# Kernel tuning notes

Measured on AMD Instinct MI355X. Metric: run time of the kernel, lower is better.

The kernel has to match this reference:

```python
import jax, jax.numpy as jnp
import numpy as np

B, N, K, S_IN, S_OUT, C, FD = 32, 325, 20, 12, 12, 10, 64
ALPHA = 0.5  # LeakyReLU negative slope

def leaky(x):
    return jnp.where(x >= 0, x, ALPHA * x)

def setup_inputs() -> dict:
    key = jax.random.key(0)
    ks = jax.random.split(key, 9)
    s = 0.2
    return {
        "fushed_features": jax.random.normal(ks[0], (B, N, FD), jnp.float32),
        "input_data": jax.random.normal(ks[1], (B, N, S_IN), jnp.float32),
        "w_W": jax.random.normal(ks[2], (S_IN, S_OUT), jnp.float32) * s,
        "w_b": jax.random.normal(ks[3], (S_OUT,), jnp.float32) * s,
        "a1_W": jax.random.normal(ks[4], (2 * S_OUT, 4 * S_OUT), jnp.float32) * s,
        "a1_b": jax.random.normal(ks[5], (4 * S_OUT,), jnp.float32) * s,
        "a2_W": jax.random.normal(ks[6], (4 * S_OUT, C), jnp.float32) * s,
        "a2_b": jax.random.normal(ks[7], (C,), jnp.float32) * s,
        "adj_mx_topk_index": jax.random.randint(ks[8], (B, N, K), 0, N),
    }

def reference(fushed_features, input_data, w_W, w_b, a1_W, a1_b, a2_W, a2_b, adj_mx_topk_index):
    # w_net: Linear + LeakyReLU -> wh [B,N,S_OUT]
    wh = leaky(input_data @ w_W + w_b)
    # a_net on cat([wh_i, wh_j]): split first linear to avoid materializing [B,N,N,2*S_OUT]
    hx = wh @ a1_W[:S_OUT]   # contribution of wh_x (row node i)
    hy = wh @ a1_W[S_OUT:]   # contribution of wh_y (col node j)
    hidden = leaky(hx[:, :, None, :] + hy[:, None, :, :] + a1_b)   # [B,N,N,4*S_OUT]
    attention = leaky(hidden @ a2_W + a2_b)                        # [B,N,N,C]
    idx = adj_mx_topk_index                                        # [B,N,K]
    # gather top-k neighbors along dim 2
    idx_c = jnp.broadcast_to(idx[..., None], idx.shape + (attention.shape[-1],))
    attention_mask = jnp.take_along_axis(attention, idx_c, axis=2)  # [B,N,K,C]
    attention_mask = jax.nn.softmax(attention_mask, axis=-1)
    # gather neighbor features: wh_expand_top_k[b,i,k] = wh[b, idx[b,i,k]]
    wh_topk = wh[jnp.arange(wh.shape[0])[:, None, None], idx]       # [B,N,K,S_OUT]
    # output = attention_mask^T @ wh_topk
    output_data = jnp.einsum('bnkc,bnks->bncs', attention_mask, wh_topk)
    # clustering loss on detached neighbor features (cosine similarity)
    wt = jax.lax.stop_gradient(wh_topk)
    wtn = wt / (jnp.linalg.norm(wt, axis=-1, keepdims=True) + 1e-8)
    dist_mat = jnp.einsum('bnks,bnls->bnkl', wtn, wtn)              # [B,N,K,K]
    same = (dist_mat >= 0.5).astype(dist_mat.dtype)
    diff = 1.0 - same
    prob = jnp.einsum('bnkc,bnlc->bnkl', attention_mask, attention_mask)
    prob = jnp.clip(prob, 1e-4, 1.0 - 1e-4)
    logp = jnp.log(prob)
    cl = -(same * logp - diff * logp)
    cluster_loss = (cl.sum((-1, -2)) - jnp.trace(cl, axis1=-2, axis2=-1)).mean()
    return output_data, cluster_loss, dist_mat.mean(), wh.mean()
```

## Files before the change

kernel.cpp:

```cpp
#include <hip/hip_runtime.h>
#include <math.h>

#define Bdim 32
#define Ndim 325
#define Kdim 20
#define Sdim 12
#define Cdim 10
#define Hdim 48
#define NB   (Bdim*Ndim)
#define OUT_SCALARS (NB*Cdim*Sdim)
#define Tpairs (Kdim*(Kdim-1)/2)
#define BN_BLOCKS (NB/4)
#define NODE_BLOCKS 260
#define NPB 40

#define O_WH  0
#define O_HX  (O_WH + NB*Sdim)
#define O_HY  (O_HX + NB*Hdim)
#define O_PCL (O_HY + NB*Hdim)
#define O_PDS (O_PCL + BN_BLOCKS)
#define O_PWH (O_PDS + BN_BLOCKS)
#define WS_BASE_FLOATS (O_PWH + NODE_BLOCKS)

__device__ __forceinline__ float leaky(float x) { return x >= 0.f ? x : 0.5f * x; }

__global__ __launch_bounds__(256)
void node_kernel(const float* __restrict__ x,
                 const float* __restrict__ wW, const float* __restrict__ wb,
                 const float* __restrict__ A1, const float* __restrict__ b1,
                 float* __restrict__ ws)
{
    __shared__ float s_wh[NPB][Sdim];
    __shared__ float s_r[4];
    const int tid = threadIdx.x;
    const int base = blockIdx.x * NPB;

    float v = 0.f;
    #pragma unroll
    for (int rep = 0; rep < 2; rep++) {
        const int e = tid + rep * 256;
        if (e < NPB * Sdim) {
            const int n = e / Sdim, s = e - n * Sdim;
            const float* xr = x + (size_t)(base + n) * Sdim;
            float acc = wb[s];
            #pragma unroll
            for (int i = 0; i < Sdim; i++) acc += xr[i] * wW[i * Sdim + s];
            acc = leaky(acc);
            s_wh[n][s] = acc;
            ws[O_WH + (size_t)(base + n) * Sdim + s] = acc;
            v += acc;
        }
    }
    __syncthreads();

    #pragma unroll
    for (int rep = 0; rep < 15; rep++) {
        const int e = tid + rep * 256;
        const int n = e / 96, r = e - n * 96;
        const int which = r / Hdim, d = r - which * Hdim;
        const float4 w0 = *(const float4*)&s_wh[n][0];
        const float4 w1 = *(const float4*)&s_wh[n][4];
        const float4 w2 = *(const float4*)&s_wh[n][8];
        const float* Ac = A1 + (which * Sdim) * Hdim + d;
        float acc = which ? 0.f : b1[d];
        acc += w0.x*Ac[0*Hdim] + w0.y*Ac[1*Hdim] + w0.z*Ac[2*Hdim] + w0.w*Ac[3*Hdim]
             + w1.x*Ac[4*Hdim] + w1.y*Ac[5*Hdim] + w1.z*Ac[6*Hdim] + w1.w*Ac[7*Hdim]
             + w2.x*Ac[8*Hdim] + w2.y*Ac[9*Hdim] + w2.z*Ac[10*Hdim] + w2.w*Ac[11*Hdim];
        ws[(which ? O_HY : O_HX) + (size_t)(base + n) * Hdim + d] = acc;
    }

    #pragma unroll
    for (int off = 32; off > 0; off >>= 1) v += __shfl_down(v, off);
    if ((tid & 63) == 0) s_r[tid >> 6] = v;
    __syncthreads();
    if (tid == 0) ws[O_PWH + blockIdx.x] = s_r[0] + s_r[1] + s_r[2] + s_r[3];
}

__global__ __launch_bounds__(256)
void mega_kernel(const int* __restrict__ topk,
                 const float* __restrict__ A2, const float* __restrict__ b2,
                 float* __restrict__ ws, float* __restrict__ out)
{
    __shared__ float s_A2  [Hdim * Cdim];
    __shared__ float s_whj [4][Kdim][12];
    __shared__ float s_am  [4][Kdim][12];
    __shared__ float s_invn[4][Kdim];
    __shared__ float s_red[2][4];

    const int tid = threadIdx.x;
    const int slot = tid >> 6, t = tid & 63;

    if (tid < 120) *(float4*)&s_A2[tid * 4] = *(const float4*)&A2[tid * 4];
    __syncthreads();

    if (tid < 160) {
        const int e = tid >> 1, half = tid & 1;
        const int gid = blockIdx.x * 80 + e;
        const int bn_e = gid / Kdim;
        const int b_e  = bn_e / Ndim;
        const int j    = topk[gid];
        const int ek   = e / 20, kk = e - ek * 20;

        const float4* hx4 = (const float4*)(ws + O_HX + (size_t)bn_e * Hdim) + half * 6;
        const float4* hy4 = (const float4*)(ws + O_HY + ((size_t)b_e * Ndim + j) * Hdim) + half * 6;

        float acc[Cdim];
        #pragma unroll
        for (int c = 0; c < Cdim; c++) acc[c] = 0.f;
        #pragma unroll
        for (int q = 0; q < 6; q++) {
            const float4 xv = hx4[q], yv = hy4[q];
            const float hh[4] = { leaky(xv.x + yv.x), leaky(xv.y + yv.y),
                                  leaky(xv.z + yv.z), leaky(xv.w + yv.w) };
            #pragma unroll
            for (int i = 0; i < 4; i++) {
                const int d = half * 24 + q * 4 + i;
                #pragma unroll
                for (int c = 0; c < Cdim; c++)
                    acc[c] += hh[i] * s_A2[d * Cdim + c];
            }
        }
        float full[Cdim];
        #pragma unroll
        for (int c = 0; c < Cdim; c++) full[c] = acc[c] + __shfl_xor(acc[c], 1);
        if (half == 0) {
            float m = -1e30f;
            #pragma unroll
            for (int c = 0; c < Cdim; c++) { full[c] = leaky(full[c] + b2[c]); m = fmaxf(m, full[c]); }
            float sum = 0.f;
            #pragma unroll
            for (int c = 0; c < Cdim; c++) { full[c] = __expf(full[c] - m); sum += full[c]; }
            const float inv = 1.f / sum;
            *(float4*)&s_am[ek][kk][0] = make_float4(full[0]*inv, full[1]*inv, full[2]*inv, full[3]*inv);
            *(float4*)&s_am[ek][kk][4] = make_float4(full[4]*inv, full[5]*inv, full[6]*inv, full[7]*inv);
            *(float4*)&s_am[ek][kk][8] = make_float4(full[8]*inv, full[9]*inv, 0.f, 0.f);
        }
    } else {
        for (int i = tid - 160; i < 240; i += 96) {
            const int kf = i / 3, q = i - kf * 3;
            const int sl = kf / 20, k = kf - sl * 20;
            const int gidx = blockIdx.x * 80 + kf;
            const int bn_i = gidx / Kdim;
            const int b_i  = bn_i / Ndim;
            const int j    = topk[gidx];
            const float4 v = *(const float4*)(ws + O_WH + ((size_t)b_i * Ndim + j) * Sdim + q * 4);
            *(float4*)&s_whj[sl][k][q * 4] = v;
        }
    }
    __syncthreads();

    const int bn = blockIdx.x * 4 + slot;
    float cl = 0.f, ds = 0.f;

    if (t < Kdim) {
        const float4 w0 = *(const float4*)&s_whj[slot][t][0];
        const float4 w1 = *(const float4*)&s_whj[slot][t][4];
        const float4 w2 = *(const float4*)&s_whj[slot][t][8];
        const float nn = w0.x*w0.x + w0.y*w0.y + w0.z*w0.z + w0.w*w0.w
                       + w1.x*w1.x + w1.y*w1.y + w1.z*w1.z + w1.w*w1.w
                       + w2.x*w2.x + w2.y*w2.y + w2.z*w2.z + w2.w*w2.w;
        const float invn = 1.f / (sqrtf(nn) + 1e-8f);
        s_invn[slot][t] = invn;
        ds += nn * invn * invn;
    } else if (t < Kdim + 30) {
        const int e = t - Kdim, c = e / 3, sq = e - c * 3;
        float4 o = make_float4(0.f, 0.f, 0.f, 0.f);
        #pragma unroll
        for (int k = 0; k < Kdim; k++) {
            const float a = s_am[slot][k][c];
            const float4 w = *(const float4*)&s_whj[slot][k][sq * 4];
            o.x += a * w.x; o.y += a * w.y; o.z += a * w.z; o.w += a * w.w;
        }
        *(float4*)(out + (size_t)bn * (Cdim * Sdim) + c * Sdim + sq * 4) = o;
    }
    __builtin_amdgcn_wave_barrier();

    #pragma unroll
    for (int it = 0; it < 3; it++) {
        const int e = t + it * 64;
        if (e < Tpairs) {
            const int r = Tpairs - 1 - e;
            const int m = (int)((sqrtf((float)(8 * r + 1)) - 1.f) * 0.5f + 1e-4f);
            const int k = Kdim - 2 - m;
            const int l = Kdim - 1 - (r - (m * (m + 1)) / 2);

            const float4 a0 = *(const float4*)&s_whj[slot][k][0];
            const float4 a1 = *(const float4*)&s_whj[slot][k][4];
            const float4 a2 = *(const float4*)&s_whj[slot][k][8];
            const float4 c0 = *(const float4*)&s_whj[slot][l][0];
            const float4 c1 = *(const float4*)&s_whj[slot][l][4];
            const float4 c2 = *(const float4*)&s_whj[slot][l][8];
            const float draw = a0.x*c0.x + a0.y*c0.y + a0.z*c0.z + a0.w*c0.w
                             + a1.x*c1.x + a1.y*c1.y + a1.z*c1.z + a1.w*c1.w
                             + a2.x*c2.x + a2.y*c2.y + a2.z*c2.z + a2.w*c2.w;
            const float d = draw * s_invn[slot][k] * s_invn[slot][l];

            const float4 p0 = *(const float4*)&s_am[slot][k][0];
            const float4 p1 = *(const float4*)&s_am[slot][k][4];
            const float4 p2 = *(const float4*)&s_am[slot][k][8];
            const float4 q0 = *(const float4*)&s_am[slot][l][0];
            const float4 q1 = *(const float4*)&s_am[slot][l][4];
            const float4 q2 = *(const float4*)&s_am[slot][l][8];
            float p = p0.x*q0.x + p0.y*q0.y + p0.z*q0.z + p0.w*q0.w
                    + p1.x*q1.x + p1.y*q1.y + p1.z*q1.z + p1.w*q1.w
                    + p2.x*q2.x + p2.y*q2.y + p2.z*q2.z + p2.w*q2.w;

            p = fminf(fmaxf(p, 1e-4f), 1.f - 1e-4f);
            const float lp = __logf(p);
            ds += 2.f * d;
            cl += 2.f * ((d >= 0.5f) ? -lp : lp);
        }
    }

    #pragma unroll
    for (int off = 32; off > 0; off >>= 1) {
        cl += __shfl_down(cl, off);
        ds += __shfl_down(ds, off);
    }
    if (t == 0) { s_red[0][slot] = cl; s_red[1][slot] = ds; }
    __syncthreads();
    if (tid == 0) {
        ws[O_PCL + blockIdx.x] = s_red[0][0] + s_red[0][1] + s_red[0][2] + s_red[0][3];
        ws[O_PDS + blockIdx.x] = s_red[1][0] + s_red[1][1] + s_red[1][2] + s_red[1][3];
    }
}

__global__ __launch_bounds__(1024)
void finalize(const float* __restrict__ ws, float* __restrict__ out)
{
    const int t = threadIdx.x;
    float cl = 0.f, ds = 0.f, wm = 0.f;
    for (int i = t; i < BN_BLOCKS; i += 1024) {
        cl += ws[O_PCL + i]; ds += ws[O_PDS + i];
    }
    if (t < NODE_BLOCKS) wm = ws[O_PWH + t];
    #pragma unroll
    for (int off = 32; off > 0; off >>= 1) {
        cl += __shfl_down(cl, off);
        ds += __shfl_down(ds, off);
        wm += __shfl_down(wm, off);
    }
    __shared__ float r[3][16];
    const int w = t >> 6, lane = t & 63;
    if (lane == 0) { r[0][w] = cl; r[1][w] = ds; r[2][w] = wm; }
    __syncthreads();
    if (t == 0) {
        float c = 0.f, d = 0.f, m = 0.f;
        #pragma unroll
        for (int i = 0; i < 16; i++) { c += r[0][i]; d += r[1][i]; m += r[2][i]; }
        out[OUT_SCALARS + 0] = c * (1.f / (float)NB);
        out[OUT_SCALARS + 1] = d * (1.f / ((float)NB * Kdim * Kdim));
        out[OUT_SCALARS + 2] = m * (1.f / ((float)NB * Sdim));
    }
}

__global__ void zero_scalars(float* out) {
    const int t = threadIdx.x;
    if (t < 3) out[OUT_SCALARS + t] = 0.f;
}

__global__ __launch_bounds__(64)
void fused_kernel(const float* __restrict__ input_data,
                  const float* __restrict__ w_W,  const float* __restrict__ w_b,
                  const float* __restrict__ a1_W, const float* __restrict__ a1_b,
                  const float* __restrict__ a2_W, const float* __restrict__ a2_b,
                  const int*   __restrict__ topk,
                  float* __restrict__ out)
{
    __shared__ float s_wW[Sdim * Sdim];
    __shared__ float s_wb[Sdim];
    __shared__ float s_A1[2 * Sdim * Hdim];
    __shared__ float s_b1[Hdim];
    __shared__ float s_A2f[Hdim * Cdim];
    __shared__ float s_b2f[Cdim];
    __shared__ float s_whs[Sdim];
    __shared__ float s_hx[Hdim];
    __shared__ float s_whj[Kdim][Sdim + 1];
    __shared__ float s_hid[Kdim][Hdim + 1];
    __shared__ float s_am [Kdim][Cdim + 1];
    __shared__ float s_wtn[Kdim][Sdim + 1];
    __shared__ int   s_idx[Kdim];

    const int t = threadIdx.x, bn = blockIdx.x, b = bn / Ndim;

    for (int i = t; i < Sdim * Sdim; i += 64)      s_wW[i] = w_W[i];
    if (t < Sdim)                                  s_wb[t] = w_b[t];
    for (int i = t; i < 2 * Sdim * Hdim; i += 64)  s_A1[i] = a1_W[i];
    if (t < Hdim)                                  s_b1[t] = a1_b[t];
    for (int i = t; i < Hdim * Cdim; i += 64)      s_A2f[i] = a2_W[i];
    if (t < Cdim)                                  s_b2f[t] = a2_b[t];
    if (t < Kdim)                                  s_idx[t] = topk[(size_t)bn * Kdim + t];
    __syncthreads();

    const float* xs = input_data + (size_t)bn * Sdim;
    if (t < Sdim) {
        float acc = s_wb[t];
        #pragma unroll
        for (int i = 0; i < Sdim; i++) acc += xs[i] * s_wW[i * Sdim + t];
        s_whs[t] = leaky(acc);
    }
    __syncthreads();

    if (t < Hdim) {
        float acc = 0.f;
        #pragma unroll
        for (int s = 0; s < Sdim; s++) acc += s_whs[s] * s_A1[s * Hdim + t];
        s_hx[t] = acc;
    }
    for (int e = t; e < Kdim * Sdim; e += 64) {
        const int k = e / Sdim, ss = e - k * Sdim;
        const float* xj = input_data + ((size_t)b * Ndim + s_idx[k]) * Sdim;
        float acc = s_wb[ss];
        #pragma unroll
        for (int i = 0; i < Sdim; i++) acc += xj[i] * s_wW[i * Sdim + ss];
        s_whj[k][ss] = leaky(acc);
    }
    __syncthreads();

    for (int e = t; e < Kdim * Hdim; e += 64) {
        const int k = e / Hdim, d = e - k * Hdim;
        float acc = s_hx[d] + s_b1[d];
        #pragma unroll
        for (int s = 0; s < Sdim; s++) acc += s_whj[k][s] * s_A1[(Sdim + s) * Hdim + d];
        s_hid[k][d] = leaky(acc);
    }
    __syncthreads();

    for (int e = t; e < Kdim * Cdim; e += 64) {
        const int k = e / Cdim, c = e - k * Cdim;
        float acc = s_b2f[c];
        #pragma unroll
        for (int d = 0; d < Hdim; d++) acc += s_hid[k][d] * s_A2f[d * Cdim + c];
        s_am[k][c] = leaky(acc);
    }
    __syncthreads();

    if (t < Kdim) {
        float m = -1e30f;
        #pragma unroll
        for (int c = 0; c < Cdim; c++) m = fmaxf(m, s_am[t][c]);
        float ex[Cdim]; float sum = 0.f;
        #pragma unroll
        for (int c = 0; c < Cdim; c++) { ex[c] = expf(s_am[t][c] - m); sum += ex[c]; }
        const float inv = 1.f / sum;
        #pragma unroll
        for (int c = 0; c < Cdim; c++) s_am[t][c] = ex[c] * inv;
        float nn = 0.f;
        #pragma unroll
        for (int s = 0; s < Sdim; s++) nn += s_whj[t][s] * s_whj[t][s];
        const float invn = 1.f / (sqrtf(nn) + 1e-8f);
        #pragma unroll
        for (int s = 0; s < Sdim; s++) s_wtn[t][s] = s_whj[t][s] * invn;
    }
    __syncthreads();

    float* op = out + (size_t)bn * (Cdim * Sdim);
    for (int e = t; e < Cdim * Sdim; e += 64) {
        const int c = e / Sdim, ss = e - c * Sdim;
        float acc = 0.f;
        #pragma unroll
        for (int k = 0; k < Kdim; k++) acc += s_am[k][c] * s_whj[k][ss];
        op[e] = acc;
    }

    float cl = 0.f, ds = 0.f;
    for (int e = t; e < Kdim * Kdim; e += 64) {
        const int k = e / Kdim, l = e - k * Kdim;
        float d = 0.f;
        #pragma unroll
        for (int s = 0; s < Sdim; s++) d += s_wtn[k][s] * s_wtn[l][s];
        ds += d;
        if (k != l) {
            float p = 0.f;
            #pragma unroll
            for (int c = 0; c < Cdim; c++) p += s_am[k][c] * s_am[l][c];
            p = fminf(fmaxf(p, 1e-4f), 1.f - 1e-4f);
            const float lp = logf(p);
            cl += (d >= 0.5f) ? -lp : lp;
        }
    }
    float whl = (t < Sdim) ? s_whs[t] : 0.f;
    #pragma unroll
    for (int off = 32; off > 0; off >>= 1) {
        cl  += __shfl_down(cl,  off);
        ds  += __shfl_down(ds,  off);
        whl += __shfl_down(whl, off);
    }
    if (t == 0) {
        atomicAdd(&out[OUT_SCALARS + 0], cl  * (1.f / (float)NB));
        atomicAdd(&out[OUT_SCALARS + 1], ds  * (1.f / ((float)NB * Kdim * Kdim)));
        atomicAdd(&out[OUT_SCALARS + 2], whl * (1.f / ((float)NB * Sdim)));
    }
}

extern "C" void kernel_launch(void* const* d_in, const int* in_sizes, int n_in,
                              void* d_out, int out_size, void* d_ws, size_t ws_size,
                              hipStream_t stream) {
    (void)in_sizes; (void)n_in; (void)out_size;
    const float* input_data = (const float*)d_in[1];
    const float* w_W  = (const float*)d_in[2];
    const float* w_b  = (const float*)d_in[3];
    const float* a1_W = (const float*)d_in[4];
    const float* a1_b = (const float*)d_in[5];
    const float* a2_W = (const float*)d_in[6];
    const float* a2_b = (const float*)d_in[7];
    const int*   topk = (const int*)d_in[8];
    float* out = (float*)d_out;
    float* ws  = (float*)d_ws;

    if (ws_size >= (size_t)WS_BASE_FLOATS * sizeof(float)) {
        hipLaunchKernelGGL(node_kernel, dim3(NODE_BLOCKS), dim3(256), 0, stream,
                           input_data, w_W, w_b, a1_W, a1_b, ws);
        hipLaunchKernelGGL(mega_kernel, dim3(BN_BLOCKS), dim3(256), 0, stream,
                           topk, a2_W, a2_b, ws, out);
        hipLaunchKernelGGL(finalize, dim3(1), dim3(1024), 0, stream, ws, out);
    } else {
        hipLaunchKernelGGL(zero_scalars, dim3(1), dim3(64), 0, stream, out);
        hipLaunchKernelGGL(fused_kernel, dim3(NB), dim3(64), 0, stream,
                           input_data, w_W, w_b, a1_W, a1_b, a2_W, a2_b, topk, out);
    }
}
```

Baseline: 103.8 us.

## Fuse node projections into mega kernel and recompute neighbor features on the fly

Drops the separate node kernel and its global wh/hx/hy buffers. Each block of the main kernel now stages all weights in shared memory and recomputes wh for its 4 nodes and their 80 top-k neighbors. It computes hx per node and hy per neighbor pair inline. Block 0 also recomputes the global wh mean across all nodes. This removes a kernel launch and several MB of intermediate global writes and gathers, in exchange for redundant FMA work per pair and a long serial tail on block 0.

```diff
diff --git a/kernel.cpp b/kernel.cpp
--- a/kernel.cpp
+++ b/kernel.cpp
@@ -11,114 +11,132 @@
 #define OUT_SCALARS (NB*Cdim*Sdim)
 #define Tpairs (Kdim*(Kdim-1)/2)
 #define BN_BLOCKS (NB/4)
-#define NODE_BLOCKS 260
-#define NPB 40
-
-#define O_WH  0
-#define O_HX  (O_WH + NB*Sdim)
-#define O_HY  (O_HX + NB*Hdim)
-#define O_PCL (O_HY + NB*Hdim)
+
+#define O_PCL 0
 #define O_PDS (O_PCL + BN_BLOCKS)
 #define O_PWH (O_PDS + BN_BLOCKS)
-#define WS_BASE_FLOATS (O_PWH + NODE_BLOCKS)
+#define WS_BASE_FLOATS (O_PWH + 4)
 
 __device__ __forceinline__ float leaky(float x) { return x >= 0.f ? x : 0.5f * x; }
 
 __global__ __launch_bounds__(256)
-void node_kernel(const float* __restrict__ x,
+void mega_kernel(const float* __restrict__ x,
                  const float* __restrict__ wW, const float* __restrict__ wb,
                  const float* __restrict__ A1, const float* __restrict__ b1,
-                 float* __restrict__ ws)
-{
-    __shared__ float s_wh[NPB][Sdim];
-    __shared__ float s_r[4];
-    const int tid = threadIdx.x;
-    const int base = blockIdx.x * NPB;
-
-    float v = 0.f;
-    #pragma unroll
-    for (int rep = 0; rep < 2; rep++) {
-        const int e = tid + rep * 256;
-        if (e < NPB * Sdim) {
-            const int n = e / Sdim, s = e - n * Sdim;
-            const float* xr = x + (size_t)(base + n) * Sdim;
-            float acc = wb[s];
-            #pragma unroll
-            for (int i = 0; i < Sdim; i++) acc += xr[i] * wW[i * Sdim + s];
-            acc = leaky(acc);
-            s_wh[n][s] = acc;
-            ws[O_WH + (size_t)(base + n) * Sdim + s] = acc;
-            v += acc;
-        }
-    }
-    __syncthreads();
-
-    #pragma unroll
-    for (int rep = 0; rep < 15; rep++) {
-        const int e = tid + rep * 256;
-        const int n = e / 96, r = e - n * 96;
-        const int which = r / Hdim, d = r - which * Hdim;
-        const float4 w0 = *(const float4*)&s_wh[n][0];
-        const float4 w1 = *(const float4*)&s_wh[n][4];
-        const float4 w2 = *(const float4*)&s_wh[n][8];
-        const float* Ac = A1 + (which * Sdim) * Hdim + d;
-        float acc = which ? 0.f : b1[d];
-        acc += w0.x*Ac[0*Hdim] + w0.y*Ac[1*Hdim] + w0.z*Ac[2*Hdim] + w0.w*Ac[3*Hdim]
-             + w1.x*Ac[4*Hdim] + w1.y*Ac[5*Hdim] + w1.z*Ac[6*Hdim] + w1.w*Ac[7*Hdim]
-             + w2.x*Ac[8*Hdim] + w2.y*Ac[9*Hdim] + w2.z*Ac[10*Hdim] + w2.w*Ac[11*Hdim];
-        ws[(which ? O_HY : O_HX) + (size_t)(base + n) * Hdim + d] = acc;
-    }
-
-    #pragma unroll
-    for (int off = 32; off > 0; off >>= 1) v += __shfl_down(v, off);
-    if ((tid & 63) == 0) s_r[tid >> 6] = v;
-    __syncthreads();
-    if (tid == 0) ws[O_PWH + blockIdx.x] = s_r[0] + s_r[1] + s_r[2] + s_r[3];
-}
-
-__global__ __launch_bounds__(256)
-void mega_kernel(const int* __restrict__ topk,
                  const float* __restrict__ A2, const float* __restrict__ b2,
+                 const int*   __restrict__ topk,
                  float* __restrict__ ws, float* __restrict__ out)
 {
-    __shared__ float s_A2  [Hdim * Cdim];
-    __shared__ float s_whj [4][Kdim][12];
-    __shared__ float s_am  [4][Kdim][12];
-    __shared__ float s_invn[4][Kdim];
+    __shared__ __attribute__((aligned(16))) float s_A1[2 * Sdim * Hdim];
+    __shared__ __attribute__((aligned(16))) float s_A2[Hdim * Cdim];
+    __shared__ __attribute__((aligned(16))) float s_wW[Sdim * Sdim];
+    __shared__ __attribute__((aligned(16))) float s_b1[Hdim];
+    __shared__ __attribute__((aligned(16))) float s_wb[Sdim];
+    __shared__ __attribute__((aligned(16))) float s_b2[12];
+    __shared__ __attribute__((aligned(16))) float s_whs[4][Sdim];
+    __shared__ __attribute__((aligned(16))) float s_hx [4][Hdim];
+    __shared__ __attribute__((aligned(16))) float s_whj[4][Kdim][12];
+    __shared__ __attribute__((aligned(16))) float s_am [4][Kdim][12];
+    __shared__ __attribute__((aligned(16))) float s_invn[4][Kdim];
     __shared__ float s_red[2][4];
+    __shared__ float s_red2[4];
 
     const int tid = threadIdx.x;
     const int slot = tid >> 6, t = tid & 63;
 
-    if (tid < 120) *(float4*)&s_A2[tid * 4] = *(const float4*)&A2[tid * 4];
+    {
+        const float4* A1_4 = (const float4*)A1;
+        const float4* A2_4 = (const float4*)A2;
+        const float4* wW_4 = (const float4*)wW;
+        const float4* b1_4 = (const float4*)b1;
+        const float4* wb_4 = (const float4*)wb;
+        for (int i = tid; i < 459; i += 256) {
+            if (i < 288)      *(float4*)&s_A1[i * 4]         = A1_4[i];
+            else if (i < 408) *(float4*)&s_A2[(i - 288) * 4] = A2_4[i - 288];
+            else if (i < 444) *(float4*)&s_wW[(i - 408) * 4] = wW_4[i - 408];
+            else if (i < 456) *(float4*)&s_b1[(i - 444) * 4] = b1_4[i - 444];
+            else              *(float4*)&s_wb[(i - 456) * 4] = wb_4[i - 456];
+        }
+        if (tid < Cdim) s_b2[tid] = b2[tid];
+    }
+    __syncthreads();
+
+    if (tid < 84) {
+        int sl, k = 0;
+        const float* xr;
+        if (tid < 80) {
+            sl = tid / 20; k = tid - sl * 20;
+            const int bn_e = blockIdx.x * 4 + sl;
+            const int b_e  = bn_e / Ndim;
+            const int j    = topk[(size_t)blockIdx.x * 80 + tid];
+            xr = x + ((size_t)b_e * Ndim + j) * Sdim;
+        } else {
+            sl = tid - 80;
+            xr = x + (size_t)(blockIdx.x * 4 + sl) * Sdim;
+        }
+        const float4 x0 = ((const float4*)xr)[0];
+        const float4 x1 = ((const float4*)xr)[1];
+        const float4 x2 = ((const float4*)xr)[2];
+        const float xs[12] = { x0.x,x0.y,x0.z,x0.w, x1.x,x1.y,x1.z,x1.w, x2.x,x2.y,x2.z,x2.w };
+        float wh[12];
+        #pragma unroll
+        for (int s = 0; s < Sdim; s++) {
+            float acc = s_wb[s];
+            #pragma unroll
+            for (int i = 0; i < Sdim; i++) acc += xs[i] * s_wW[i * Sdim + s];
+            wh[s] = leaky(acc);
+        }
+        float* dst = (tid < 80) ? &s_whj[sl][k][0] : &s_whs[sl][0];
+        ((float4*)dst)[0] = make_float4(wh[0], wh[1], wh[2],  wh[3]);
+        ((float4*)dst)[1] = make_float4(wh[4], wh[5], wh[6],  wh[7]);
+        ((float4*)dst)[2] = make_float4(wh[8], wh[9], wh[10], wh[11]);
+    }
+    __syncthreads();
+
+    float cl = 0.f, ds = 0.f;
+
+    if (tid < 192) {
+        const int sl = tid / Hdim, d = tid - sl * Hdim;
+        float acc = s_b1[d];
+        #pragma unroll
+        for (int s = 0; s < Sdim; s++) acc += s_whs[sl][s] * s_A1[s * Hdim + d];
+        s_hx[sl][d] = acc;
+    } else {
+        for (int i = tid - 192; i < 80; i += 64) {
+            const int sl = i / 20, k = i - sl * 20;
+            const float4 w0 = *(const float4*)&s_whj[sl][k][0];
+            const float4 w1 = *(const float4*)&s_whj[sl][k][4];
+            const float4 w2 = *(const float4*)&s_whj[sl][k][8];
+            const float nn = w0.x*w0.x + w0.y*w0.y + w0.z*w0.z + w0.w*w0.w
+                           + w1.x*w1.x + w1.y*w1.y + w1.z*w1.z + w1.w*w1.w
+                           + w2.x*w2.x + w2.y*w2.y + w2.z*w2.z + w2.w*w2.w;
+            const float invn = 1.f / (sqrtf(nn) + 1e-8f);
+            s_invn[sl][k] = invn;
+            ds += nn * invn * invn;
+        }
+    }
     __syncthreads();
 
     if (tid < 160) {
         const int e = tid >> 1, half = tid & 1;
-        const int gid = blockIdx.x * 80 + e;
-        const int bn_e = gid / Kdim;
-        const int b_e  = bn_e / Ndim;
-        const int j    = topk[gid];
-        const int ek   = e / 20, kk = e - ek * 20;
-
-        const float4* hx4 = (const float4*)(ws + O_HX + (size_t)bn_e * Hdim) + half * 6;
-        const float4* hy4 = (const float4*)(ws + O_HY + ((size_t)b_e * Ndim + j) * Hdim) + half * 6;
+        const int sl = e / 20, kk = e - sl * 20;
+        const float4 w0 = *(const float4*)&s_whj[sl][kk][0];
+        const float4 w1 = *(const float4*)&s_whj[sl][kk][4];
+        const float4 w2 = *(const float4*)&s_whj[sl][kk][8];
+        const float w[12] = { w0.x,w0.y,w0.z,w0.w, w1.x,w1.y,w1.z,w1.w, w2.x,w2.y,w2.z,w2.w };
 
         float acc[Cdim];
         #pragma unroll
         for (int c = 0; c < Cdim; c++) acc[c] = 0.f;
         #pragma unroll
-        for (int q = 0; q < 6; q++) {
-            const float4 xv = hx4[q], yv = hy4[q];
-            const float hh[4] = { leaky(xv.x + yv.x), leaky(xv.y + yv.y),
-                                  leaky(xv.z + yv.z), leaky(xv.w + yv.w) };
-            #pragma unroll
-            for (int i = 0; i < 4; i++) {
-                const int d = half * 24 + q * 4 + i;
-                #pragma unroll
-                for (int c = 0; c < Cdim; c++)
-                    acc[c] += hh[i] * s_A2[d * Cdim + c];
-            }
+        for (int dd = 0; dd < 24; dd++) {
+            const int d = half * 24 + dd;
+            float hy = 0.f;
+            #pragma unroll
+            for (int s = 0; s < Sdim; s++) hy += w[s] * s_A1[(Sdim + s) * Hdim + d];
+            const float h = leaky(s_hx[sl][d] + hy);
+            #pragma unroll
+            for (int c = 0; c < Cdim; c++) acc[c] += h * s_A2[d * Cdim + c];
         }
         float full[Cdim];
         #pragma unroll
@@ -126,54 +144,31 @@
         if (half == 0) {
             float m = -1e30f;
             #pragma unroll
-            for (int c = 0; c < Cdim; c++) { full[c] = leaky(full[c] + b2[c]); m = fmaxf(m, full[c]); }
+            for (int c = 0; c < Cdim; c++) { full[c] = leaky(full[c] + s_b2[c]); m = fmaxf(m, full[c]); }
             float sum = 0.f;
             #pragma unroll
             for (int c = 0; c < Cdim; c++) { full[c] = __expf(full[c] - m); sum += full[c]; }
             const float inv = 1.f / sum;
-            *(float4*)&s_am[ek][kk][0] = make_float4(full[0]*inv, full[1]*inv, full[2]*inv, full[3]*inv);
-            *(float4*)&s_am[ek][kk][4] = make_float4(full[4]*inv, full[5]*inv, full[6]*inv, full[7]*inv);
-            *(float4*)&s_am[ek][kk][8] = make_float4(full[8]*inv, full[9]*inv, 0.f, 0.f);
-        }
-    } else {
-        for (int i = tid - 160; i < 240; i += 96) {
-            const int kf = i / 3, q = i - kf * 3;
-            const int sl = kf / 20, k = kf - sl * 20;
-            const int gidx = blockIdx.x * 80 + kf;
-            const int bn_i = gidx / Kdim;
-            const int b_i  = bn_i / Ndim;
-            const int j    = topk[gidx];
-            const float4 v = *(const float4*)(ws + O_WH + ((size_t)b_i * Ndim + j) * Sdim + q * 4);
-            *(float4*)&s_whj[sl][k][q * 4] = v;
+            *(float4*)&s_am[sl][kk][0] = make_float4(full[0]*inv, full[1]*inv, full[2]*inv, full[3]*inv);
+            *(float4*)&s_am[sl][kk][4] = make_float4(full[4]*inv, full[5]*inv, full[6]*inv, full[7]*inv);
+            *(float4*)&s_am[sl][kk][8] = make_float4(full[8]*inv, full[9]*inv, 0.f, 0.f);
         }
     }
     __syncthreads();
 
     const int bn = blockIdx.x * 4 + slot;
-    float cl = 0.f, ds = 0.f;
-
-    if (t < Kdim) {
-        const float4 w0 = *(const float4*)&s_whj[slot][t][0];
-        const float4 w1 = *(const float4*)&s_whj[slot][t][4];
-        const float4 w2 = *(const float4*)&s_whj[slot][t][8];
-        const float nn = w0.x*w0.x + w0.y*w0.y + w0.z*w0.z + w0.w*w0.w
-                       + w1.x*w1.x + w1.y*w1.y + w1.z*w1.z + w1.w*w1.w
-                       + w2.x*w2.x + w2.y*w2.y + w2.z*w2.z + w2.w*w2.w;
-        const float invn = 1.f / (sqrtf(nn) + 1e-8f);
-        s_invn[slot][t] = invn;
-        ds += nn * invn * invn;
-    } else if (t < Kdim + 30) {
-        const int e = t - Kdim, c = e / 3, sq = e - c * 3;
+
+    if (t < 30) {
+        const int c = t / 3, sq = t - c * 3;
         float4 o = make_float4(0.f, 0.f, 0.f, 0.f);
         #pragma unroll
         for (int k = 0; k < Kdim; k++) {
             const float a = s_am[slot][k][c];
-            const float4 w = *(const float4*)&s_whj[slot][k][sq * 4];
-            o.x += a * w.x; o.y += a * w.y; o.z += a * w.z; o.w += a * w.w;
+            const float4 wv = *(const float4*)&s_whj[slot][k][sq * 4];
+            o.x += a * wv.x; o.y += a * wv.y; o.z += a * wv.z; o.w += a * wv.w;
         }
         *(float4*)(out + (size_t)bn * (Cdim * Sdim) + c * Sdim + sq * 4) = o;
     }
-    __builtin_amdgcn_wave_barrier();
 
     #pragma unroll
     for (int it = 0; it < 3; it++) {
@@ -223,17 +218,40 @@
         ws[O_PCL + blockIdx.x] = s_red[0][0] + s_red[0][1] + s_red[0][2] + s_red[0][3];
         ws[O_PDS + blockIdx.x] = s_red[1][0] + s_red[1][1] + s_red[1][2] + s_red[1][3];
     }
+
+    if (blockIdx.x == 0) {
+        float wm = 0.f;
+        for (int node = tid; node < NB; node += 256) {
+            const float* xr = x + (size_t)node * Sdim;
+            const float4 x0 = ((const float4*)xr)[0];
+            const float4 x1 = ((const float4*)xr)[1];
+            const float4 x2 = ((const float4*)xr)[2];
+            const float xs[12] = { x0.x,x0.y,x0.z,x0.w, x1.x,x1.y,x1.z,x1.w, x2.x,x2.y,x2.z,x2.w };
+            #pragma unroll
+            for (int s = 0; s < Sdim; s++) {
+                float acc = s_wb[s];
+                #pragma unroll
+                for (int i = 0; i < Sdim; i++) acc += xs[i] * s_wW[i * Sdim + s];
+                wm += leaky(acc);
+            }
+        }
+        #pragma unroll
+        for (int off = 32; off > 0; off >>= 1) wm += __shfl_down(wm, off);
+        if (t == 0) s_red2[slot] = wm;
+        __syncthreads();
+        if (tid == 0) ws[O_PWH] = s_red2[0] + s_red2[1] + s_red2[2] + s_red2[3];
+    }
 }
 
 __global__ __launch_bounds__(1024)
 void finalize(const float* __restrict__ ws, float* __restrict__ out)
 {
     const int t = threadIdx.x;
-    float cl = 0.f, ds = 0.f, wm = 0.f;
+    float cl = 0.f, ds = 0.f;
+    float wm = (t == 0) ? ws[O_PWH] : 0.f;
     for (int i = t; i < BN_BLOCKS; i += 1024) {
         cl += ws[O_PCL + i]; ds += ws[O_PDS + i];
     }
-    if (t < NODE_BLOCKS) wm = ws[O_PWH + t];
     #pragma unroll
     for (int off = 32; off > 0; off >>= 1) {
         cl += __shfl_down(cl, off);
@@ -409,10 +427,8 @@
     float* ws  = (float*)d_ws;
 
     if (ws_size >= (size_t)WS_BASE_FLOATS * sizeof(float)) {
-        hipLaunchKernelGGL(node_kernel, dim3(NODE_BLOCKS), dim3(256), 0, stream,
-                           input_data, w_W, w_b, a1_W, a1_b, ws);
         hipLaunchKernelGGL(mega_kernel, dim3(BN_BLOCKS), dim3(256), 0, stream,
-                           topk, a2_W, a2_b, ws, out);
+                           input_data, w_W, w_b, a1_W, a1_b, a2_W, a2_b, topk, ws, out);
         hipLaunchKernelGGL(finalize, dim3(1), dim3(1024), 0, stream, ws, out);
     } else {
         hipLaunchKernelGGL(zero_scalars, dim3(1), dim3(64), 0, stream, out);
```

Result: slower. 150.1 us (+44.6%).
